# Optimization experiments

Measured on AMD Instinct MI355X. Metric: run time of the kernel, lower is better.

The kernel has to match this reference:

```python
import jax, jax.numpy as jnp
import numpy as np

N, NFEAT, NHID, NH2, NCLASS = 16384, 512, 256, 64, 10


def setup_inputs() -> dict:
    key = jax.random.key(0)
    ks = jax.random.split(key, 12)
    x = jax.random.normal(ks[0], (N, NFEAT), dtype=jnp.float32)
    # dense (row-normalized-style) adjacency; sparsified to ~avg degree 32
    a = jax.random.uniform(ks[1], (N, N), dtype=jnp.float32)
    mask = (jax.random.uniform(ks[2], (N, N)) < (32.0 / N)).astype(jnp.float32)
    adj = a * mask / 32.0
    s = lambda fin: 1.0 / np.sqrt(fin)
    W1 = jax.random.uniform(ks[3], (NFEAT, NHID), jnp.float32, -s(NFEAT), s(NFEAT))
    b1 = jax.random.uniform(ks[4], (NHID,), jnp.float32, -s(NFEAT), s(NFEAT))
    W2 = jax.random.uniform(ks[5], (NHID, NH2), jnp.float32, -s(NHID), s(NHID))
    b2 = jax.random.uniform(ks[6], (NH2,), jnp.float32, -s(NHID), s(NHID))
    W3 = jax.random.uniform(ks[7], (NH2, 32), jnp.float32, -s(NH2), s(NH2))
    b3 = jax.random.uniform(ks[8], (32,), jnp.float32, -s(NH2), s(NH2))
    W4 = jax.random.uniform(ks[9], (32, 16), jnp.float32, -s(32), s(32))
    b4 = jax.random.uniform(ks[10], (16,), jnp.float32, -s(32), s(32))
    W5 = jax.random.uniform(ks[11], (16, NCLASS), jnp.float32, -s(16), s(16))
    b5 = jnp.zeros((NCLASS,), jnp.float32)
    return {"x": x, "adj": adj, "W1": W1, "b1": b1, "W2": W2, "b2": b2,
            "W3": W3, "b3": b3, "W4": W4, "b4": b4, "W5": W5, "b5": b5}


def reference(x, adj, W1, b1, W2, b2, W3, b3, W4, b4, W5, b5):
    # GraphConvolution: adj @ (x @ W) + b
    h = jax.nn.relu(adj @ (x @ W1) + b1)          # [N, NHID]
    h = adj @ (h @ W2) + b2                        # [N, 64]
    g = jnp.max(h, axis=0)                         # [64] graph max-pool
    g = jax.nn.relu(g @ W3 + b3)                   # [32]
    g = jax.nn.relu(g @ W4 + b4)                   # [16]
    return g @ W5 + b5                             # [NCLASS]
```

## Files before the change

kernel.cpp:

```cpp
#include <hip/hip_runtime.h>
#include <hip/hip_bf16.h>
#include <cstdint>

#define NROW 16384
#define NFEAT 512
#define NHID 256
#define NH2 64
#define CAP 96

#define GM 64
#define GN 64
#define GK 16
__global__ __launch_bounds__(256) void gemm_xw1(const float* __restrict__ X,
                                                const float* __restrict__ W,
                                                float* __restrict__ out) {
    __shared__ float As[GK][GM + 1];
    __shared__ float Bs[GK][GN];
    const int tid = threadIdx.x;
    const int bm = blockIdx.y * GM;
    const int bn = blockIdx.x * GN;
    const int tx = tid % 16, ty = tid / 16;
    float acc[4][4] = {};
    for (int k0 = 0; k0 < NFEAT; k0 += GK) {
        {
            int m = tid / 4;
            int kk = (tid % 4) * 4;
            const float4 v = *(const float4*)&X[(size_t)(bm + m) * NFEAT + k0 + kk];
            As[kk + 0][m] = v.x; As[kk + 1][m] = v.y;
            As[kk + 2][m] = v.z; As[kk + 3][m] = v.w;
        }
        {
            int kk = tid / 16;
            int n = (tid % 16) * 4;
            const float4 v = *(const float4*)&W[(size_t)(k0 + kk) * NHID + bn + n];
            *(float4*)&Bs[kk][n] = v;
        }
        __syncthreads();
#pragma unroll
        for (int k = 0; k < GK; ++k) {
            float a[4], b[4];
#pragma unroll
            for (int i = 0; i < 4; ++i) a[i] = As[k][ty * 4 + i];
#pragma unroll
            for (int j = 0; j < 4; ++j) b[j] = Bs[k][tx * 4 + j];
#pragma unroll
            for (int i = 0; i < 4; ++i)
#pragma unroll
                for (int j = 0; j < 4; ++j) acc[i][j] += a[i] * b[j];
        }
        __syncthreads();
    }
#pragma unroll
    for (int i = 0; i < 4; ++i) {
        float4 v = {acc[i][0], acc[i][1], acc[i][2], acc[i][3]};
        *(float4*)&out[(size_t)(bm + ty * 4 + i) * NHID + bn + tx * 4] = v;
    }
}

__global__ __launch_bounds__(256) void build_csr(const float* __restrict__ adj,
                                                 float* __restrict__ vals,
                                                 int* __restrict__ cols,
                                                 int* __restrict__ cnt) {
    const int wave = threadIdx.x / 64;
    const int lane = threadIdx.x % 64;
    const int row = blockIdx.x * 4 + wave;
    const float* arow = adj + (size_t)row * NROW;
    int count = 0;
    for (int c0 = 0; c0 < NROW; c0 += 256) {
        const float4 v = *(const float4*)&arow[c0 + lane * 4];
#pragma unroll
        for (int k = 0; k < 4; ++k) {
            float val = (k == 0) ? v.x : (k == 1) ? v.y : (k == 2) ? v.z : v.w;
            unsigned long long m = __ballot(val != 0.0f);
            if (val != 0.0f) {
                int pos = count + __popcll(m & ((1ull << lane) - 1ull));
                if (pos < CAP) {
                    vals[(size_t)row * CAP + pos] = val;
                    cols[(size_t)row * CAP + pos] = c0 + lane * 4 + k;
                }
            }
            count += __popcll(m);
        }
    }
    if (lane == 0) cnt[row] = count < CAP ? count : CAP;
}

__global__ __launch_bounds__(256) void prop1(const float* __restrict__ XW1,
                                             const float* __restrict__ vals,
                                             const int* __restrict__ cols,
                                             const int* __restrict__ cnt,
                                             const float* __restrict__ b1,
                                             float* __restrict__ H1) {
    const int row = blockIdx.x;
    const int c = threadIdx.x;
    const int n = cnt[row];
    const float* v = vals + (size_t)row * CAP;
    const int* cl = cols + (size_t)row * CAP;
    float acc = 0.f;
    for (int k = 0; k < n; ++k)
        acc += v[k] * XW1[(size_t)cl[k] * NHID + c];
    acc += b1[c];
    H1[(size_t)row * NHID + c] = acc > 0.f ? acc : 0.f;
}

__global__ __launch_bounds__(256) void gemm_h1w2(const float* __restrict__ H1,
                                                 const float* __restrict__ W2,
                                                 float* __restrict__ out) {
    const int gid = blockIdx.x * 256 + threadIdx.x;
    const int i = gid / NH2;
    const int c = gid % NH2;
    const float* h = H1 + (size_t)i * NHID;
    float acc = 0.f;
#pragma unroll 4
    for (int k = 0; k < NHID; ++k) acc += h[k] * W2[k * NH2 + c];
    out[(size_t)i * NH2 + c] = acc;
}

__global__ __launch_bounds__(64) void prop2(const float* __restrict__ H1W2,
                                            const float* __restrict__ vals,
                                            const int* __restrict__ cols,
                                            const int* __restrict__ cnt,
                                            const float* __restrict__ b2,
                                            float* __restrict__ H2) {
    const int row = blockIdx.x;
    const int c = threadIdx.x;
    const int n = cnt[row];
    const float* v = vals + (size_t)row * CAP;
    const int* cl = cols + (size_t)row * CAP;
    float acc = 0.f;
    for (int k = 0; k < n; ++k)
        acc += v[k] * H1W2[(size_t)cl[k] * NH2 + c];
    H2[(size_t)row * NH2 + c] = acc + b2[c];
}

__global__ __launch_bounds__(256) void colmax(const float* __restrict__ H2,
                                              float* __restrict__ partial) {
    __shared__ float sm[256];
    const int t = threadIdx.x;
    const int c = t % 64, r0 = t / 64;
    const int base = blockIdx.x * 256;
    float m = -3.4e38f;
    for (int r = r0; r < 256; r += 4) {
        float v = H2[(size_t)(base + r) * NH2 + c];
        m = v > m ? v : m;
    }
    sm[t] = m;
    __syncthreads();
    if (t < 64) {
        float mm = fmaxf(fmaxf(sm[t], sm[t + 64]), fmaxf(sm[t + 128], sm[t + 192]));
        partial[blockIdx.x * 64 + t] = mm;
    }
}

__global__ __launch_bounds__(64) void final_mlp(const float* __restrict__ partial,
                                                const float* __restrict__ W3,
                                                const float* __restrict__ b3,
                                                const float* __restrict__ W4,
                                                const float* __restrict__ b4,
                                                const float* __restrict__ W5,
                                                const float* __restrict__ b5,
                                                float* __restrict__ out) {
    __shared__ float g[64], t3[32], t4[16];
    const int t = threadIdx.x;
    float m = -3.4e38f;
    for (int p = 0; p < 64; ++p) m = fmaxf(m, partial[p * 64 + t]);
    g[t] = m;
    __syncthreads();
    if (t < 32) {
        float acc = b3[t];
        for (int k = 0; k < 64; ++k) acc += g[k] * W3[k * 32 + t];
        t3[t] = acc > 0.f ? acc : 0.f;
    }
    __syncthreads();
    if (t < 16) {
        float acc = b4[t];
        for (int k = 0; k < 32; ++k) acc += t3[k] * W4[k * 16 + t];
        t4[t] = acc > 0.f ? acc : 0.f;
    }
    __syncthreads();
    if (t < 10) {
        float acc = b5[t];
        for (int k = 0; k < 16; ++k) acc += t4[k] * W5[k * 10 + t];
        out[t] = acc;
    }
}

extern "C" void kernel_launch(void* const* d_in, const int* in_sizes, int n_in,
                              void* d_out, int out_size, void* d_ws, size_t ws_size,
                              hipStream_t stream) {
    const float* x   = (const float*)d_in[0];
    const float* adj = (const float*)d_in[1];
    const float* W1  = (const float*)d_in[2];
    const float* b1  = (const float*)d_in[3];
    const float* W2  = (const float*)d_in[4];
    const float* b2  = (const float*)d_in[5];
    const float* W3  = (const float*)d_in[6];
    const float* b3  = (const float*)d_in[7];
    const float* W4  = (const float*)d_in[8];
    const float* b4  = (const float*)d_in[9];
    const float* W5  = (const float*)d_in[10];
    const float* b5  = (const float*)d_in[11];
    float* out = (float*)d_out;

    char* ws = (char*)d_ws;
    float* XW1   = (float*)(ws);
    float* H1    = (float*)(ws + (size_t)16777216);
    float* H1W2  = (float*)(ws + (size_t)33554432);
    float* H2    = (float*)(ws + (size_t)37748736);
    float* vals  = (float*)(ws + (size_t)41943040);
    int*   cols  = (int*)  (ws + (size_t)48234496);
    int*   cnt   = (int*)  (ws + (size_t)54525952);
    float* part  = (float*)(ws + (size_t)54591488);

    build_csr<<<NROW / 4, 256, 0, stream>>>(adj, vals, cols, cnt);
    dim3 g1(NHID / GN, NROW / GM);
    gemm_xw1<<<g1, 256, 0, stream>>>(x, W1, XW1);
    prop1<<<NROW, 256, 0, stream>>>(XW1, vals, cols, cnt, b1, H1);
    gemm_h1w2<<<NROW * NH2 / 256, 256, 0, stream>>>(H1, W2, H1W2);
    prop2<<<NROW, 64, 0, stream>>>(H1W2, vals, cols, cnt, b2, H2);
    colmax<<<64, 256, 0, stream>>>(H2, part);
    final_mlp<<<1, 64, 0, stream>>>(part, W3, b3, W4, b4, W5, b5, out);
}
```

Before: 1.670 ms.

## Fuse CSR build with XW1 GEMM, fold H1·W2 into prop1, pool in prop2

Merges the CSR-building pass and the X·W1 GEMM into one launch, with block-index ranges deciding which job each block does, and enlarges the GEMM tile to 128x64. Fuses the first propagation with the H1·W2 product through shared memory, so H1 is never written to global memory, and stages the CSR rows in LDS. Fuses the second propagation with a per-block column max, so H2 is never materialised. The intent is to cut launches and large intermediate round-trips through HBM. The cost is a heavier kernel with more LDS, and each prop1 block now handles four rows in sequence, which can lower parallelism in the latency-bound gather.

```diff
diff --git a/kernel.cpp b/kernel.cpp
--- a/kernel.cpp
+++ b/kernel.cpp
@@ -8,216 +8,252 @@
 #define NH2 64
 #define CAP 96
 
-#define GM 64
-#define GN 64
-#define GK 16
-__global__ __launch_bounds__(256) void gemm_xw1(const float* __restrict__ X,
-                                                const float* __restrict__ W,
-                                                float* __restrict__ out) {
-    __shared__ float As[GK][GM + 1];
-    __shared__ float Bs[GK][GN];
-    const int tid = threadIdx.x;
-    const int bm = blockIdx.y * GM;
-    const int bn = blockIdx.x * GN;
-    const int tx = tid % 16, ty = tid / 16;
-    float acc[4][4] = {};
-    for (int k0 = 0; k0 < NFEAT; k0 += GK) {
-        {
-            int m = tid / 4;
-            int kk = (tid % 4) * 4;
-            const float4 v = *(const float4*)&X[(size_t)(bm + m) * NFEAT + k0 + kk];
-            As[kk + 0][m] = v.x; As[kk + 1][m] = v.y;
-            As[kk + 2][m] = v.z; As[kk + 3][m] = v.w;
-        }
-        {
-            int kk = tid / 16;
-            int n = (tid % 16) * 4;
-            const float4 v = *(const float4*)&W[(size_t)(k0 + kk) * NHID + bn + n];
-            *(float4*)&Bs[kk][n] = v;
-        }
-        __syncthreads();
-#pragma unroll
-        for (int k = 0; k < GK; ++k) {
-            float a[4], b[4];
-#pragma unroll
-            for (int i = 0; i < 4; ++i) a[i] = As[k][ty * 4 + i];
-#pragma unroll
-            for (int j = 0; j < 4; ++j) b[j] = Bs[k][tx * 4 + j];
-#pragma unroll
-            for (int i = 0; i < 4; ++i)
-#pragma unroll
-                for (int j = 0; j < 4; ++j) acc[i][j] += a[i] * b[j];
-        }
-        __syncthreads();
-    }
-#pragma unroll
-    for (int i = 0; i < 4; ++i) {
-        float4 v = {acc[i][0], acc[i][1], acc[i][2], acc[i][3]};
-        *(float4*)&out[(size_t)(bm + ty * 4 + i) * NHID + bn + tx * 4] = v;
-    }
-}
-
-__global__ __launch_bounds__(256) void build_csr(const float* __restrict__ adj,
-                                                 float* __restrict__ vals,
-                                                 int* __restrict__ cols,
-                                                 int* __restrict__ cnt) {
-    const int wave = threadIdx.x / 64;
-    const int lane = threadIdx.x % 64;
-    const int row = blockIdx.x * 4 + wave;
+#define BM 128
+#define BN 64
+#define BK 16
+#define GEMM_BLOCKS 512
+
+__global__ __launch_bounds__(256, 4) void k0_csr_gemm(
+    const float* __restrict__ X, const float* __restrict__ W1,
+    const float* __restrict__ adj,
+    float* __restrict__ XW1, float* __restrict__ vals,
+    int* __restrict__ cols, int* __restrict__ cnt) {
+  __shared__ float As[BK][BM + 4];
+  __shared__ float Bs[BK][BN];
+  const int t = threadIdx.x;
+
+  if (blockIdx.x < GEMM_BLOCKS) {
+    const int bm = (blockIdx.x >> 2) * BM;
+    const int bn = (blockIdx.x & 3) * BN;
+    const int tx = t & 15;
+    const int ty = t >> 4;
+    const int ar = t >> 1;
+    const int ak = (t & 1) * 8;
+    const int bk = t >> 4;
+    const int bnn = (t & 15) * 4;
+    float acc[8][4] = {};
+    for (int k0 = 0; k0 < NFEAT; k0 += BK) {
+      const float4 a0 = *(const float4*)&X[(size_t)(bm + ar) * NFEAT + k0 + ak];
+      const float4 a1 = *(const float4*)&X[(size_t)(bm + ar) * NFEAT + k0 + ak + 4];
+      const float4 b0 = *(const float4*)&W1[(size_t)(k0 + bk) * NHID + bn + bnn];
+      As[ak + 0][ar] = a0.x; As[ak + 1][ar] = a0.y;
+      As[ak + 2][ar] = a0.z; As[ak + 3][ar] = a0.w;
+      As[ak + 4][ar] = a1.x; As[ak + 5][ar] = a1.y;
+      As[ak + 6][ar] = a1.z; As[ak + 7][ar] = a1.w;
+      *(float4*)&Bs[bk][bnn] = b0;
+      __syncthreads();
+#pragma unroll
+      for (int k = 0; k < BK; ++k) {
+        float a[8], b[4];
+#pragma unroll
+        for (int i = 0; i < 8; ++i) a[i] = As[k][ty * 8 + i];
+#pragma unroll
+        for (int j = 0; j < 4; ++j) b[j] = Bs[k][tx * 4 + j];
+#pragma unroll
+        for (int i = 0; i < 8; ++i)
+#pragma unroll
+          for (int j = 0; j < 4; ++j) acc[i][j] += a[i] * b[j];
+      }
+      __syncthreads();
+    }
+#pragma unroll
+    for (int i = 0; i < 8; ++i) {
+      float4 v = {acc[i][0], acc[i][1], acc[i][2], acc[i][3]};
+      *(float4*)&XW1[(size_t)(bm + ty * 8 + i) * NHID + bn + tx * 4] = v;
+    }
+  } else {
+    const int wave = t >> 6;
+    const int lane = t & 63;
+    const int row = (blockIdx.x - GEMM_BLOCKS) * 4 + wave;
     const float* arow = adj + (size_t)row * NROW;
     int count = 0;
     for (int c0 = 0; c0 < NROW; c0 += 256) {
-        const float4 v = *(const float4*)&arow[c0 + lane * 4];
-#pragma unroll
-        for (int k = 0; k < 4; ++k) {
-            float val = (k == 0) ? v.x : (k == 1) ? v.y : (k == 2) ? v.z : v.w;
-            unsigned long long m = __ballot(val != 0.0f);
-            if (val != 0.0f) {
-                int pos = count + __popcll(m & ((1ull << lane) - 1ull));
-                if (pos < CAP) {
-                    vals[(size_t)row * CAP + pos] = val;
-                    cols[(size_t)row * CAP + pos] = c0 + lane * 4 + k;
-                }
-            }
-            count += __popcll(m);
+      const float4 v = *(const float4*)&arow[c0 + lane * 4];
+#pragma unroll
+      for (int k = 0; k < 4; ++k) {
+        const float val = (k == 0) ? v.x : (k == 1) ? v.y : (k == 2) ? v.z : v.w;
+        const unsigned long long m = __ballot(val != 0.0f);
+        if (val != 0.0f) {
+          const int pos = count + __popcll(m & ((1ull << lane) - 1ull));
+          if (pos < CAP) {
+            vals[(size_t)row * CAP + pos] = val;
+            cols[(size_t)row * CAP + pos] = c0 + lane * 4 + k;
+          }
         }
+        count += __popcll(m);
+      }
     }
     if (lane == 0) cnt[row] = count < CAP ? count : CAP;
-}
-
-__global__ __launch_bounds__(256) void prop1(const float* __restrict__ XW1,
-                                             const float* __restrict__ vals,
-                                             const int* __restrict__ cols,
-                                             const int* __restrict__ cnt,
-                                             const float* __restrict__ b1,
-                                             float* __restrict__ H1) {
-    const int row = blockIdx.x;
-    const int c = threadIdx.x;
-    const int n = cnt[row];
-    const float* v = vals + (size_t)row * CAP;
-    const int* cl = cols + (size_t)row * CAP;
-    float acc = 0.f;
-    for (int k = 0; k < n; ++k)
-        acc += v[k] * XW1[(size_t)cl[k] * NHID + c];
-    acc += b1[c];
-    H1[(size_t)row * NHID + c] = acc > 0.f ? acc : 0.f;
-}
-
-__global__ __launch_bounds__(256) void gemm_h1w2(const float* __restrict__ H1,
-                                                 const float* __restrict__ W2,
-                                                 float* __restrict__ out) {
-    const int gid = blockIdx.x * 256 + threadIdx.x;
-    const int i = gid / NH2;
-    const int c = gid % NH2;
-    const float* h = H1 + (size_t)i * NHID;
-    float acc = 0.f;
-#pragma unroll 4
-    for (int k = 0; k < NHID; ++k) acc += h[k] * W2[k * NH2 + c];
-    out[(size_t)i * NH2 + c] = acc;
-}
-
-__global__ __launch_bounds__(64) void prop2(const float* __restrict__ H1W2,
-                                            const float* __restrict__ vals,
-                                            const int* __restrict__ cols,
-                                            const int* __restrict__ cnt,
-                                            const float* __restrict__ b2,
-                                            float* __restrict__ H2) {
-    const int row = blockIdx.x;
-    const int c = threadIdx.x;
-    const int n = cnt[row];
-    const float* v = vals + (size_t)row * CAP;
-    const int* cl = cols + (size_t)row * CAP;
-    float acc = 0.f;
-    for (int k = 0; k < n; ++k)
-        acc += v[k] * H1W2[(size_t)cl[k] * NH2 + c];
-    H2[(size_t)row * NH2 + c] = acc + b2[c];
-}
-
-__global__ __launch_bounds__(256) void colmax(const float* __restrict__ H2,
-                                              float* __restrict__ partial) {
-    __shared__ float sm[256];
-    const int t = threadIdx.x;
-    const int c = t % 64, r0 = t / 64;
-    const int base = blockIdx.x * 256;
-    float m = -3.4e38f;
-    for (int r = r0; r < 256; r += 4) {
-        float v = H2[(size_t)(base + r) * NH2 + c];
-        m = v > m ? v : m;
-    }
-    sm[t] = m;
-    __syncthreads();
-    if (t < 64) {
-        float mm = fmaxf(fmaxf(sm[t], sm[t + 64]), fmaxf(sm[t + 128], sm[t + 192]));
-        partial[blockIdx.x * 64 + t] = mm;
-    }
-}
-
-__global__ __launch_bounds__(64) void final_mlp(const float* __restrict__ partial,
-                                                const float* __restrict__ W3,
-                                                const float* __restrict__ b3,
-                                                const float* __restrict__ W4,
-                                                const float* __restrict__ b4,
-                                                const float* __restrict__ W5,
-                                                const float* __restrict__ b5,
-                                                float* __restrict__ out) {
-    __shared__ float g[64], t3[32], t4[16];
-    const int t = threadIdx.x;
-    float m = -3.4e38f;
-    for (int p = 0; p < 64; ++p) m = fmaxf(m, partial[p * 64 + t]);
-    g[t] = m;
-    __syncthreads();
-    if (t < 32) {
-        float acc = b3[t];
-        for (int k = 0; k < 64; ++k) acc += g[k] * W3[k * 32 + t];
-        t3[t] = acc > 0.f ? acc : 0.f;
-    }
-    __syncthreads();
-    if (t < 16) {
-        float acc = b4[t];
-        for (int k = 0; k < 32; ++k) acc += t3[k] * W4[k * 16 + t];
-        t4[t] = acc > 0.f ? acc : 0.f;
-    }
-    __syncthreads();
-    if (t < 10) {
-        float acc = b5[t];
-        for (int k = 0; k < 16; ++k) acc += t4[k] * W5[k * 10 + t];
-        out[t] = acc;
-    }
+  }
+}
+
+__global__ __launch_bounds__(256, 4) void k1_prop1(
+    const float* __restrict__ XW1, const float* __restrict__ vals,
+    const int* __restrict__ cols, const int* __restrict__ cnt,
+    const float* __restrict__ b1, const float* __restrict__ W2,
+    float* __restrict__ H1W2) {
+  __shared__ int   scl[4][CAP];
+  __shared__ float sv[4][CAP];
+  __shared__ float sh[4][NHID];
+  __shared__ float sp[4][256];
+  const int t = threadIdx.x;
+  const int row0 = blockIdx.x * 4;
+  {
+    const int r = t >> 6, j = t & 63;
+    const int n = cnt[row0 + r];
+    for (int jj = j; jj < n; jj += 64) {
+      scl[r][jj] = cols[(size_t)(row0 + r) * CAP + jj];
+      sv[r][jj]  = vals[(size_t)(row0 + r) * CAP + jj];
+    }
+  }
+  __syncthreads();
+  const float bias = b1[t];
+  for (int r = 0; r < 4; ++r) {
+    const int n = cnt[row0 + r];
+    float a0 = 0.f, a1 = 0.f, a2 = 0.f, a3 = 0.f;
+    int k = 0;
+    for (; k + 4 <= n; k += 4) {
+      a0 += sv[r][k + 0] * XW1[(size_t)scl[r][k + 0] * NHID + t];
+      a1 += sv[r][k + 1] * XW1[(size_t)scl[r][k + 1] * NHID + t];
+      a2 += sv[r][k + 2] * XW1[(size_t)scl[r][k + 2] * NHID + t];
+      a3 += sv[r][k + 3] * XW1[(size_t)scl[r][k + 3] * NHID + t];
+    }
+    for (; k < n; ++k) a0 += sv[r][k] * XW1[(size_t)scl[r][k] * NHID + t];
+    const float h = a0 + a1 + a2 + a3 + bias;
+    sh[r][t] = h > 0.f ? h : 0.f;
+  }
+  __syncthreads();
+  const int c = t & 63, q = t >> 6;
+  float p0 = 0.f, p1 = 0.f, p2 = 0.f, p3 = 0.f;
+#pragma unroll 8
+  for (int kk = 0; kk < 64; ++kk) {
+    const int kidx = q * 64 + kk;
+    const float w = W2[kidx * NH2 + c];
+    p0 += sh[0][kidx] * w;
+    p1 += sh[1][kidx] * w;
+    p2 += sh[2][kidx] * w;
+    p3 += sh[3][kidx] * w;
+  }
+  sp[0][t] = p0; sp[1][t] = p1; sp[2][t] = p2; sp[3][t] = p3;
+  __syncthreads();
+  {
+    const int r2 = t >> 6, c2 = t & 63;
+    H1W2[(size_t)(row0 + r2) * NH2 + c2] =
+        sp[r2][c2] + sp[r2][c2 + 64] + sp[r2][c2 + 128] + sp[r2][c2 + 192];
+  }
+}
+
+__global__ __launch_bounds__(256, 4) void k2_prop2(
+    const float* __restrict__ H1W2, const float* __restrict__ vals,
+    const int* __restrict__ cols, const int* __restrict__ cnt,
+    const float* __restrict__ b2, float* __restrict__ blockmax) {
+  __shared__ int   scl[4][CAP];
+  __shared__ float sv[4][CAP];
+  __shared__ float smax[4][NH2];
+  const int t = threadIdx.x;
+  const int w = t >> 6, l = t & 63;
+  const int row = blockIdx.x * 4 + w;
+  const int n = cnt[row];
+  for (int jj = l; jj < n; jj += 64) {
+    scl[w][jj] = cols[(size_t)row * CAP + jj];
+    sv[w][jj]  = vals[(size_t)row * CAP + jj];
+  }
+  __syncthreads();
+  float a0 = 0.f, a1 = 0.f, a2 = 0.f, a3 = 0.f;
+  int k = 0;
+  for (; k + 4 <= n; k += 4) {
+    a0 += sv[w][k + 0] * H1W2[(size_t)scl[w][k + 0] * NH2 + l];
+    a1 += sv[w][k + 1] * H1W2[(size_t)scl[w][k + 1] * NH2 + l];
+    a2 += sv[w][k + 2] * H1W2[(size_t)scl[w][k + 2] * NH2 + l];
+    a3 += sv[w][k + 3] * H1W2[(size_t)scl[w][k + 3] * NH2 + l];
+  }
+  for (; k < n; ++k) a0 += sv[w][k] * H1W2[(size_t)scl[w][k] * NH2 + l];
+  smax[w][l] = a0 + a1 + a2 + a3 + b2[l];
+  __syncthreads();
+  if (t < NH2) {
+    const float m = fmaxf(fmaxf(smax[0][t], smax[1][t]),
+                          fmaxf(smax[2][t], smax[3][t]));
+    blockmax[(size_t)blockIdx.x * NH2 + t] = m;
+  }
+}
+
+__global__ __launch_bounds__(256) void k3_colmax(const float* __restrict__ blockmax,
+                                                 float* __restrict__ partial) {
+  __shared__ float sm[256];
+  const int t = threadIdx.x, c = t & 63, q = t >> 6;
+  const int base = blockIdx.x * 64;
+  float m = -3.4e38f;
+  for (int r = q; r < 64; r += 4)
+    m = fmaxf(m, blockmax[(size_t)(base + r) * NH2 + c]);
+  sm[t] = m;
+  __syncthreads();
+  if (t < 64)
+    partial[blockIdx.x * 64 + t] =
+        fmaxf(fmaxf(sm[t], sm[t + 64]), fmaxf(sm[t + 128], sm[t + 192]));
+}
+
+__global__ __launch_bounds__(64) void k4_final(const float* __restrict__ partial,
+                                               const float* __restrict__ W3,
+                                               const float* __restrict__ b3,
+                                               const float* __restrict__ W4,
+                                               const float* __restrict__ b4,
+                                               const float* __restrict__ W5,
+                                               const float* __restrict__ b5,
+                                               float* __restrict__ out) {
+  __shared__ float g[64], t3[32], t4[16];
+  const int t = threadIdx.x;
+  float m = -3.4e38f;
+  for (int p = 0; p < 64; ++p) m = fmaxf(m, partial[p * 64 + t]);
+  g[t] = m;
+  __syncthreads();
+  if (t < 32) {
+    float acc = b3[t];
+    for (int k = 0; k < 64; ++k) acc += g[k] * W3[k * 32 + t];
+    t3[t] = acc > 0.f ? acc : 0.f;
+  }
+  __syncthreads();
+  if (t < 16) {
+    float acc = b4[t];
+    for (int k = 0; k < 32; ++k) acc += t3[k] * W4[k * 16 + t];
+    t4[t] = acc > 0.f ? acc : 0.f;
+  }
+  __syncthreads();
+  if (t < 10) {
+    float acc = b5[t];
+    for (int k = 0; k < 16; ++k) acc += t4[k] * W5[k * 10 + t];
+    out[t] = acc;
+  }
 }
 
 extern "C" void kernel_launch(void* const* d_in, const int* in_sizes, int n_in,
                               void* d_out, int out_size, void* d_ws, size_t ws_size,
                               hipStream_t stream) {
-    const float* x   = (const float*)d_in[0];
-    const float* adj = (const float*)d_in[1];
-    const float* W1  = (const float*)d_in[2];
-    const float* b1  = (const float*)d_in[3];
-    const float* W2  = (const float*)d_in[4];
-    const float* b2  = (const float*)d_in[5];
-    const float* W3  = (const float*)d_in[6];
-    const float* b3  = (const float*)d_in[7];
-    const float* W4  = (const float*)d_in[8];
-    const float* b4  = (const float*)d_in[9];
-    const float* W5  = (const float*)d_in[10];
-    const float* b5  = (const float*)d_in[11];
-    float* out = (float*)d_out;
-
-    char* ws = (char*)d_ws;
-    float* XW1   = (float*)(ws);
-    float* H1    = (float*)(ws + (size_t)16777216);
-    float* H1W2  = (float*)(ws + (size_t)33554432);
-    float* H2    = (float*)(ws + (size_t)37748736);
-    float* vals  = (float*)(ws + (size_t)41943040);
-    int*   cols  = (int*)  (ws + (size_t)48234496);
-    int*   cnt   = (int*)  (ws + (size_t)54525952);
-    float* part  = (float*)(ws + (size_t)54591488);
-
-    build_csr<<<NROW / 4, 256, 0, stream>>>(adj, vals, cols, cnt);
-    dim3 g1(NHID / GN, NROW / GM);
-    gemm_xw1<<<g1, 256, 0, stream>>>(x, W1, XW1);
-    prop1<<<NROW, 256, 0, stream>>>(XW1, vals, cols, cnt, b1, H1);
-    gemm_h1w2<<<NROW * NH2 / 256, 256, 0, stream>>>(H1, W2, H1W2);
-    prop2<<<NROW, 64, 0, stream>>>(H1W2, vals, cols, cnt, b2, H2);
-    colmax<<<64, 256, 0, stream>>>(H2, part);
-    final_mlp<<<1, 64, 0, stream>>>(part, W3, b3, W4, b4, W5, b5, out);
-}
+  const float* x   = (const float*)d_in[0];
+  const float* adj = (const float*)d_in[1];
+  const float* W1  = (const float*)d_in[2];
+  const float* b1  = (const float*)d_in[3];
+  const float* W2  = (const float*)d_in[4];
+  const float* b2  = (const float*)d_in[5];
+  const float* W3  = (const float*)d_in[6];
+  const float* b3  = (const float*)d_in[7];
+  const float* W4  = (const float*)d_in[8];
+  const float* b4  = (const float*)d_in[9];
+  const float* W5  = (const float*)d_in[10];
+  const float* b5  = (const float*)d_in[11];
+  float* out = (float*)d_out;
+
+  char* ws = (char*)d_ws;
+  float* XW1      = (float*)(ws);
+  float* vals     = (float*)(ws + (size_t)16 * 1024 * 1024);
+  int*   cols     = (int*)  (ws + (size_t)24 * 1024 * 1024);
+  int*   cnt      = (int*)  (ws + (size_t)32 * 1024 * 1024);
+  float* H1W2     = (float*)(ws + (size_t)36 * 1024 * 1024);
+  float* blockmax = (float*)(ws + (size_t)40 * 1024 * 1024);
+  float* partial  = (float*)(ws + (size_t)44 * 1024 * 1024);
+
+  k0_csr_gemm<<<GEMM_BLOCKS + NROW / 4, 256, 0, stream>>>(x, W1, adj, XW1, vals, cols, cnt);
+  k1_prop1<<<NROW / 4, 256, 0, stream>>>(XW1, vals, cols, cnt, b1, W2, H1W2);
+  k2_prop2<<<NROW / 4, 256, 0, stream>>>(H1W2, vals, cols, cnt, b2, blockmax);
+  k3_colmax<<<64, 256, 0, stream>>>(blockmax, partial);
+  k4_final<<<1, 64, 0, stream>>>(partial, W3, b3, W4, b4, W5, b5, out);
+}
```

Result: faster. 1.499 ms (-10.2%).
